# Optimization experiments

Measured on AMD Instinct MI355X. Metric: run time of the kernel, lower is better.

## Reference

```python
import jax, jax.numpy as jnp
import numpy as np

B, N, E, H = 16, 1024, 1024, 16
D = E // H  # head size = 64

def setup_inputs() -> dict:
    key = jax.random.key(0)
    ks = jax.random.split(key, 5)
    s = 1.0 / np.sqrt(E)
    return {
        "x": jax.random.normal(ks[0], (B, N, E), dtype=jnp.float32),
        "W_qkv": jax.random.normal(ks[1], (E, 3 * E), dtype=jnp.float32) * s,
        "b_qkv": jnp.zeros((3 * E,), dtype=jnp.float32),
        "W_proj": jax.random.normal(ks[2], (E, E), dtype=jnp.float32) * s,
        "b_proj": jnp.zeros((E,), dtype=jnp.float32),
    }

def reference(x, W_qkv, b_qkv, W_proj, b_proj):
    # qkv projection: [B,N,3E]
    qkv = x @ W_qkv + b_qkv
    q, k, v = jnp.split(qkv, 3, axis=-1)
    # b n (h d) -> b h n d
    def split_heads(t):
        return t.reshape(B, N, H, D).transpose(0, 2, 1, 3)
    q, k, v = split_heads(q), split_heads(k), split_heads(v)
    scale = D ** -0.5
    attn = jnp.einsum('bhnd,bhmd->bhnm', q, k) * scale  # [B,H,N,N]
    attn = jax.nn.softmax(attn, axis=-1)
    # dropout p=0 -> identity
    o = jnp.einsum('bhnm,bhmd->bhnd', attn, v)  # [B,H,N,D]
    o = o.transpose(0, 2, 1, 3).reshape(B, N, E)  # b h n d -> b n (h d)
    return o @ W_proj + b_proj
```

## Files before the change

kernel.cpp:

```cpp
#include <hip/hip_runtime.h>
#include <hip/hip_bf16.h>
#include <math.h>

#define BB 16
#define NN 1024
#define EE 1024
#define HH 16
#define DD 64
#define THREE_E 3072
#define M_TOTAL (BB * NN)

typedef __attribute__((ext_vector_type(8))) short bf16x8;
typedef __attribute__((ext_vector_type(4))) short bf16x4;
typedef __attribute__((ext_vector_type(4))) float floatx4;

#define SCALE_Q 0.18033688011112042f

static __device__ __forceinline__ unsigned short f2bf(float f) {
    union { float f; unsigned u; } x; x.f = f;
    unsigned r = x.u + 0x7fffu + ((x.u >> 16) & 1u);
    return (unsigned short)(r >> 16);
}

static __device__ __forceinline__ bf16x8 pack8v(floatx4 a, floatx4 b) {
    union { bf16x8 v; unsigned u[4]; } r;
    __hip_bfloat162 t;
    t = __float22bfloat162_rn(make_float2(a[0], a[1])); r.u[0] = *(unsigned*)&t;
    t = __float22bfloat162_rn(make_float2(a[2], a[3])); r.u[1] = *(unsigned*)&t;
    t = __float22bfloat162_rn(make_float2(b[0], b[1])); r.u[2] = *(unsigned*)&t;
    t = __float22bfloat162_rn(make_float2(b[2], b[3])); r.u[3] = *(unsigned*)&t;
    return r.v;
}
static __device__ __forceinline__ bf16x8 pack8f(float4 a, float4 b) {
    union { bf16x8 v; unsigned u[4]; } r;
    __hip_bfloat162 t;
    t = __float22bfloat162_rn(make_float2(a.x, a.y)); r.u[0] = *(unsigned*)&t;
    t = __float22bfloat162_rn(make_float2(a.z, a.w)); r.u[1] = *(unsigned*)&t;
    t = __float22bfloat162_rn(make_float2(b.x, b.y)); r.u[2] = *(unsigned*)&t;
    t = __float22bfloat162_rn(make_float2(b.z, b.w)); r.u[3] = *(unsigned*)&t;
    return r.v;
}

#define ASYNC16(gp, lp)                                                \
    __builtin_amdgcn_global_load_lds(                                  \
        (const __attribute__((address_space(1))) void*)(gp),           \
        (__attribute__((address_space(3))) void*)(lp), 16, 0, 0)

#define DRAIN_VMEM() __asm__ __volatile__("s_waitcnt vmcnt(0)" ::: "memory")

__global__ __launch_bounds__(256) void convert_x(
    const float* __restrict__ x, unsigned short* __restrict__ xb)
{
    int i = blockIdx.x * 256 + threadIdx.x;
    const float4* xp = (const float4*)x;
    float4 a = xp[i * 2], b = xp[i * 2 + 1];
    *(bf16x8*)&xb[i * 8] = pack8f(a, b);
}

__global__ __launch_bounds__(256) void wtrans(
    const float* __restrict__ w, unsigned short* __restrict__ wt, int R, int C)
{
    __shared__ float tile[32][33];
    const int t = threadIdx.x;
    const int lr = t >> 5, lc = t & 31;
    const int r0 = blockIdx.y * 32, c0 = blockIdx.x * 32;
    #pragma unroll
    for (int p = 0; p < 4; ++p)
        tile[lr + p * 8][lc] = w[(size_t)(r0 + lr + p * 8) * C + c0 + lc];
    __syncthreads();
    #pragma unroll
    for (int p = 0; p < 4; ++p) {
        int oc = lr + p * 8;
        float v = tile[lc][oc];
        wt[(size_t)(c0 + oc) * R + r0 + lc] = f2bf(v);
    }
}

__global__ __launch_bounds__(256) void gemm_qkv_mfma(
    const unsigned short* __restrict__ xb,
    const unsigned short* __restrict__ wt,
    const float* __restrict__ bias,
    unsigned short* __restrict__ Qo, unsigned short* __restrict__ Ko,
    unsigned short* __restrict__ Vo)
{
    __shared__ __align__(16) unsigned short As[128 * 32];
    __shared__ __align__(16) unsigned short Bs[128 * 32];

    const int t = threadIdx.x;
    const int w = t >> 6, lane = t & 63;
    const int quad = lane >> 4, l15 = lane & 15;
    const int wm = w >> 1, wn = w & 1;
    const int m0 = blockIdx.y * 128;
    const int n0 = blockIdx.x * 128;
    const int srow = lane >> 2;
    const int scw = (((lane & 3) ^ ((srow ^ (srow >> 2)) & 3))) * 8;
    const int rsw = ((quad ^ ((l15 ^ (l15 >> 2)) & 3))) * 8;

    floatx4 acc[4][4];
    #pragma unroll
    for (int i = 0; i < 4; ++i)
        #pragma unroll
        for (int j = 0; j < 4; ++j) acc[i][j] = (floatx4){0.f, 0.f, 0.f, 0.f};

    for (int kk = 0; kk < EE; kk += 32) {
        #pragma unroll
        for (int r = 0; r < 2; ++r) {
            int c = w * 2 + r;
            ASYNC16(&xb[(size_t)(m0 + c * 16 + srow) * EE + kk + scw],
                    &As[c * 512]);
            ASYNC16(&wt[(size_t)(n0 + c * 16 + srow) * EE + kk + scw],
                    &Bs[c * 512]);
        }
        DRAIN_VMEM();
        __syncthreads();

        bf16x8 af[4], bf[4];
        #pragma unroll
        for (int i = 0; i < 4; ++i) {
            af[i] = *(const bf16x8*)&As[(wm * 64 + i * 16 + l15) * 32 + rsw];
            bf[i] = *(const bf16x8*)&Bs[(wn * 64 + i * 16 + l15) * 32 + rsw];
        }
        #pragma unroll
        for (int i = 0; i < 4; ++i)
            #pragma unroll
            for (int j = 0; j < 4; ++j)
                acc[i][j] = __builtin_amdgcn_mfma_f32_16x16x32_bf16(
                    af[i], bf[j], acc[i][j], 0, 0, 0);
        __syncthreads();
    }

    const int mb = m0 + wm * 64;
    const int nb = n0 + wn * 64;
    #pragma unroll
    for (int i = 0; i < 4; ++i) {
        #pragma unroll
        for (int j = 0; j < 4; ++j) {
            int nc = nb + j * 16;
            int which = nc >> 10;
            int e0 = nc & 1023;
            int h  = e0 >> 6;
            int d0 = e0 & 63;
            float bv = bias[nc + l15];
            #pragma unroll
            for (int r = 0; r < 4; ++r) {
                int m = mb + i * 16 + quad * 4 + r;
                int b = m >> 10, n = m & 1023;
                size_t off = ((size_t)(b * HH + h) * NN + n) * DD + d0 + l15;
                float v = acc[i][j][r] + bv;
                if (which == 0)      Qo[off] = f2bf(v * SCALE_Q);
                else if (which == 1) Ko[off] = f2bf(v);
                else                 Vo[off] = f2bf(v);
            }
        }
    }
}

__global__ __launch_bounds__(256) void vtrans(
    const unsigned short* __restrict__ V, unsigned short* __restrict__ Vt)
{
    __shared__ __align__(16) unsigned short tile[64][72];
    const int t  = threadIdx.x;
    const int bh = blockIdx.x;
    const int n0 = blockIdx.y * 64;
    const int r  = t >> 2, c = t & 3;

    const unsigned short* src = &V[((size_t)bh * NN + n0 + r) * DD + c * 16];
    bf16x8 v0 = *(const bf16x8*)&src[0];
    bf16x8 v1 = *(const bf16x8*)&src[8];
    #pragma unroll
    for (int k = 0; k < 8; ++k) tile[c * 16 + k][r]     = v0[k];
    #pragma unroll
    for (int k = 0; k < 8; ++k) tile[c * 16 + 8 + k][r] = v1[k];
    __syncthreads();

    unsigned short* dst = &Vt[((size_t)bh * DD + r) * NN + n0 + c * 16];
    *(bf16x8*)&dst[0] = *(const bf16x8*)&tile[r][c * 16];
    *(bf16x8*)&dst[8] = *(const bf16x8*)&tile[r][c * 16 + 8];
}

__global__ __launch_bounds__(256) void attn_mfma(
    const unsigned short* __restrict__ Q,
    const unsigned short* __restrict__ K,
    const unsigned short* __restrict__ Vt,
    unsigned short* __restrict__ O)
{
    __shared__ __align__(16) unsigned short Ks[64 * 64];
    __shared__ __align__(16) unsigned short Vs[64 * 64];

    const int t    = threadIdx.x;
    const int w    = t >> 6;
    const int quad = (t >> 4) & 3;
    const int l15  = t & 15;
    const int i    = blockIdx.x;
    const int bh   = ((i >> 6) << 3) | (i & 7);
    const int qt   = (i >> 3) & 7;

    const unsigned short* Qg = Q  + (size_t)bh * NN * DD;
    const unsigned short* Kg = K  + (size_t)bh * NN * DD;
    const unsigned short* Vg = Vt + (size_t)bh * DD * NN;

    const int q0 = qt * 128 + w * 32;

    bf16x8 qf[2][2];
    #pragma unroll
    for (int a = 0; a < 2; ++a) {
        qf[a][0] = *(const bf16x8*)&Qg[(size_t)(q0 + a * 16 + l15) * DD + quad * 8];
        qf[a][1] = *(const bf16x8*)&Qg[(size_t)(q0 + a * 16 + l15) * DD + 32 + quad * 8];
    }

    floatx4 oa[2][4];
    #pragma unroll
    for (int a = 0; a < 2; ++a)
        #pragma unroll
        for (int jd = 0; jd < 4; ++jd) oa[a][jd] = (floatx4){0.f, 0.f, 0.f, 0.f};
    float lsum[2] = {0.f, 0.f};

    const int srow = t >> 2;
    const int sc   = t & 3;
    const int swz  = srow & 7;
    const int cbase = ((quad ^ (l15 & 7)) << 3);

    bf16x8 kr0, kr1, vr0, vr1;
    {
        const unsigned short* kg = &Kg[(size_t)srow * DD + sc * 16];
        kr0 = *(const bf16x8*)&kg[0];
        kr1 = *(const bf16x8*)&kg[8];
        const unsigned short* vg = &Vg[(size_t)srow * NN + sc * 16];
        vr0 = *(const bf16x8*)&vg[0];
        vr1 = *(const bf16x8*)&vg[8];
    }

    for (int kt = 0; kt < 16; ++kt) {
        __syncthreads();
        *(bf16x8*)&Ks[srow * 64 + (((2 * sc + 0) ^ swz) << 3)] = kr0;
        *(bf16x8*)&Ks[srow * 64 + (((2 * sc + 1) ^ swz) << 3)] = kr1;
        {
            bf16x4 h[4];
            h[0] = (bf16x4){vr0[0], vr0[1], vr0[2], vr0[3]};
            h[1] = (bf16x4){vr0[4], vr0[5], vr0[6], vr0[7]};
            h[2] = (bf16x4){vr1[0], vr1[1], vr1[2], vr1[3]};
            h[3] = (bf16x4){vr1[4], vr1[5], vr1[6], vr1[7]};
            #pragma unroll
            for (int q = 0; q < 4; ++q) {
                int col = ((((sc >> 1) * 4 + q) ^ swz) << 3) + ((sc & 1) << 2);
                *(bf16x4*)&Vs[srow * 64 + col] = h[q];
            }
        }
        __syncthreads();

        if (kt < 15) {
            const unsigned short* kg =
                &Kg[(size_t)((kt + 1) * 64 + srow) * DD + sc * 16];
            kr0 = *(const bf16x8*)&kg[0];
            kr1 = *(const bf16x8*)&kg[8];
            const unsigned short* vg =
                &Vg[(size_t)srow * NN + (kt + 1) * 64 + sc * 16];
            vr0 = *(const bf16x8*)&vg[0];
            vr1 = *(const bf16x8*)&vg[8];
        }

        floatx4 sa[2][4];
        #pragma unroll
        for (int a = 0; a < 2; ++a)
            #pragma unroll
            for (int tt = 0; tt < 4; ++tt) sa[a][tt] = (floatx4){0.f, 0.f, 0.f, 0.f};
        #pragma unroll
        for (int tt = 0; tt < 4; ++tt) {
            const unsigned short* kb = &Ks[(tt * 16 + l15) * 64];
            bf16x8 kf0 = *(const bf16x8*)&kb[cbase];
            bf16x8 kf1 = *(const bf16x8*)&kb[cbase ^ 32];
            #pragma unroll
            for (int a = 0; a < 2; ++a) {
                sa[a][tt] = __builtin_amdgcn_mfma_f32_16x16x32_bf16(
                    kf0, qf[a][0], sa[a][tt], 0, 0, 0);
                sa[a][tt] = __builtin_amdgcn_mfma_f32_16x16x32_bf16(
                    kf1, qf[a][1], sa[a][tt], 0, 0, 0);
            }
        }

        bf16x8 pf[2][2];
        #pragma unroll
        for (int a = 0; a < 2; ++a) {
            floatx4 pe[4];
            #pragma unroll
            for (int tt = 0; tt < 4; ++tt) {
                #pragma unroll
                for (int r = 0; r < 4; ++r) {
                    float p = exp2f(sa[a][tt][r]);
                    pe[tt][r] = p;
                    lsum[a] += p;
                }
            }
            pf[a][0] = pack8v(pe[0], pe[1]);
            pf[a][1] = pack8v(pe[2], pe[3]);
        }

        #pragma unroll
        for (int jd = 0; jd < 4; ++jd) {
            const unsigned short* vb = &Vs[(jd * 16 + l15) * 64];
            bf16x8 vf0 = *(const bf16x8*)&vb[cbase];
            bf16x8 vf1 = *(const bf16x8*)&vb[cbase ^ 32];
            #pragma unroll
            for (int a = 0; a < 2; ++a) {
                oa[a][jd] = __builtin_amdgcn_mfma_f32_16x16x32_bf16(
                    vf0, pf[a][0], oa[a][jd], 0, 0, 0);
                oa[a][jd] = __builtin_amdgcn_mfma_f32_16x16x32_bf16(
                    vf1, pf[a][1], oa[a][jd], 0, 0, 0);
            }
        }
    }

    #pragma unroll
    for (int a = 0; a < 2; ++a) {
        lsum[a] += __shfl_xor(lsum[a], 16, 64);
        lsum[a] += __shfl_xor(lsum[a], 32, 64);
    }

    const int b = bh >> 4, h = bh & 15;
    #pragma unroll
    for (int a = 0; a < 2; ++a) {
        float inv = 1.f / lsum[a];
        int n = q0 + a * 16 + l15;
        size_t base = (size_t)(b * NN + n) * EE + h * DD;
        #pragma unroll
        for (int jd = 0; jd < 4; ++jd) {
            bf16x4 v;
            v[0] = (short)f2bf(oa[a][jd][0] * inv);
            v[1] = (short)f2bf(oa[a][jd][1] * inv);
            v[2] = (short)f2bf(oa[a][jd][2] * inv);
            v[3] = (short)f2bf(oa[a][jd][3] * inv);
            *(bf16x4*)&O[base + jd * 16 + quad * 4] = v;
        }
    }
}

__global__ __launch_bounds__(256) void gemm_proj_mfma(
    const unsigned short* __restrict__ Ob,
    const unsigned short* __restrict__ Bp,
    const float* __restrict__ bias, float* __restrict__ out)
{
    __shared__ __align__(16) unsigned short As[128 * 32];
    __shared__ __align__(16) unsigned short Bs[128 * 32];

    const int t = threadIdx.x;
    const int w = t >> 6, lane = t & 63;
    const int quad = lane >> 4, l15 = lane & 15;
    const int wm = w >> 1, wn = w & 1;
    const int m0 = blockIdx.y * 128;
    const int n0 = blockIdx.x * 128;
    const int srow = lane >> 2;
    const int scw = (((lane & 3) ^ ((srow ^ (srow >> 2)) & 3))) * 8;
    const int rsw = ((quad ^ ((l15 ^ (l15 >> 2)) & 3))) * 8;

    floatx4 acc[4][4];
    #pragma unroll
    for (int i = 0; i < 4; ++i)
        #pragma unroll
        for (int j = 0; j < 4; ++j) acc[i][j] = (floatx4){0.f, 0.f, 0.f, 0.f};

    for (int kk = 0; kk < EE; kk += 32) {
        #pragma unroll
        for (int r = 0; r < 2; ++r) {
            int c = w * 2 + r;
            ASYNC16(&Ob[(size_t)(m0 + c * 16 + srow) * EE + kk + scw],
                    &As[c * 512]);
            ASYNC16(&Bp[(size_t)(n0 + c * 16 + srow) * EE + kk + scw],
                    &Bs[c * 512]);
        }
        DRAIN_VMEM();
        __syncthreads();

        bf16x8 af[4], bf[4];
        #pragma unroll
        for (int i = 0; i < 4; ++i) {
            af[i] = *(const bf16x8*)&As[(wm * 64 + i * 16 + l15) * 32 + rsw];
            bf[i] = *(const bf16x8*)&Bs[(wn * 64 + i * 16 + l15) * 32 + rsw];
        }
        #pragma unroll
        for (int i = 0; i < 4; ++i)
            #pragma unroll
            for (int j = 0; j < 4; ++j)
                acc[i][j] = __builtin_amdgcn_mfma_f32_16x16x32_bf16(
                    af[i], bf[j], acc[i][j], 0, 0, 0);
        __syncthreads();
    }

    const int mb = m0 + wm * 64;
    const int nb = n0 + wn * 64;
    #pragma unroll
    for (int i = 0; i < 4; ++i) {
        #pragma unroll
        for (int j = 0; j < 4; ++j) {
            float bv = bias[nb + j * 16 + l15];
            #pragma unroll
            for (int r = 0; r < 4; ++r) {
                int mrow = mb + i * 16 + quad * 4 + r;
                out[(size_t)mrow * EE + nb + j * 16 + l15] = acc[i][j][r] + bv;
            }
        }
    }
}

extern "C" void kernel_launch(void* const* d_in, const int* in_sizes, int n_in,
                              void* d_out, int out_size, void* d_ws, size_t ws_size,
                              hipStream_t stream) {
    const float* x     = (const float*)d_in[0];
    const float* Wqkv  = (const float*)d_in[1];
    const float* bqkv  = (const float*)d_in[2];
    const float* Wproj = (const float*)d_in[3];
    const float* bproj = (const float*)d_in[4];
    float* out = (float*)d_out;

    const size_t BHND = (size_t)BB * HH * NN * DD;
    unsigned short* Q   = (unsigned short*)d_ws;
    unsigned short* K   = Q   + BHND;
    unsigned short* Vn  = K   + BHND;
    unsigned short* Vt  = Vn  + BHND;
    unsigned short* Ob  = Vt  + BHND;
    unsigned short* xb  = Ob  + BHND;
    unsigned short* Wqt = xb  + BHND;
    unsigned short* Wpt = Wqt + (size_t)THREE_E * EE;

    dim3 blk(256);
    convert_x<<<dim3(M_TOTAL * EE / (256 * 8)), blk, 0, stream>>>(x, xb);
    wtrans<<<dim3(THREE_E / 32, EE / 32), blk, 0, stream>>>(Wqkv, Wqt, EE, THREE_E);
    wtrans<<<dim3(EE / 32, EE / 32), blk, 0, stream>>>(Wproj, Wpt, EE, EE);

    gemm_qkv_mfma<<<dim3(THREE_E / 128, M_TOTAL / 128), blk, 0, stream>>>(
        xb, Wqt, bqkv, Q, K, Vn);
    vtrans<<<dim3(BB * HH, NN / 64), blk, 0, stream>>>(Vn, Vt);
    attn_mfma<<<dim3(BB * HH * NN / 128), blk, 0, stream>>>(Q, K, Vt, Ob);
    gemm_proj_mfma<<<dim3(EE / 128, M_TOTAL / 128), blk, 0, stream>>>(
        Ob, Wpt, bproj, out);
}
```

Measured before the change: 447.2 us.

## Double GEMM K-tile, compute softmax row sums via MFMA, use raw exp2 and setprio

```diff
diff --git a/kernel.cpp b/kernel.cpp
--- a/kernel.cpp
+++ b/kernel.cpp
@@ -20,6 +20,14 @@
     union { float f; unsigned u; } x; x.f = f;
     unsigned r = x.u + 0x7fffu + ((x.u >> 16) & 1u);
     return (unsigned short)(r >> 16);
+}
+
+static __device__ __forceinline__ float fast_exp2(float x) {
+#if __has_builtin(__builtin_amdgcn_exp2f)
+    return __builtin_amdgcn_exp2f(x);
+#else
+    float r; __asm__("v_exp_f32 %0, %1" : "=v"(r) : "v"(x)); return r;
+#endif
 }
 
 static __device__ __forceinline__ bf16x8 pack8v(floatx4 a, floatx4 b) {
@@ -83,8 +91,8 @@
     unsigned short* __restrict__ Qo, unsigned short* __restrict__ Ko,
     unsigned short* __restrict__ Vo)
 {
-    __shared__ __align__(16) unsigned short As[128 * 32];
-    __shared__ __align__(16) unsigned short Bs[128 * 32];
+    __shared__ __align__(16) unsigned short As[128 * 64];
+    __shared__ __align__(16) unsigned short Bs[128 * 64];
 
     const int t = threadIdx.x;
     const int w = t >> 6, lane = t & 63;
@@ -92,9 +100,10 @@
     const int wm = w >> 1, wn = w & 1;
     const int m0 = blockIdx.y * 128;
     const int n0 = blockIdx.x * 128;
-    const int srow = lane >> 2;
-    const int scw = (((lane & 3) ^ ((srow ^ (srow >> 2)) & 3))) * 8;
-    const int rsw = ((quad ^ ((l15 ^ (l15 >> 2)) & 3))) * 8;
+    const int srow = lane >> 3;
+    const int sch  = lane & 7;
+    const int scw  = (sch ^ srow) * 8;
+    const int rb   = l15 & 7;
 
     floatx4 acc[4][4];
     #pragma unroll
@@ -102,30 +111,34 @@
         #pragma unroll
         for (int j = 0; j < 4; ++j) acc[i][j] = (floatx4){0.f, 0.f, 0.f, 0.f};
 
-    for (int kk = 0; kk < EE; kk += 32) {
-        #pragma unroll
-        for (int r = 0; r < 2; ++r) {
-            int c = w * 2 + r;
-            ASYNC16(&xb[(size_t)(m0 + c * 16 + srow) * EE + kk + scw],
-                    &As[c * 512]);
-            ASYNC16(&wt[(size_t)(n0 + c * 16 + srow) * EE + kk + scw],
-                    &Bs[c * 512]);
+    const unsigned short* aG = &xb[(size_t)(m0 + w * 8 + srow) * EE + scw];
+    const unsigned short* bG = &wt[(size_t)(n0 + w * 8 + srow) * EE + scw];
+
+    for (int kk = 0; kk < EE; kk += 64) {
+        #pragma unroll
+        for (int p = 0; p < 4; ++p) {
+            ASYNC16(aG + kk + (size_t)(p * 32) * EE, &As[(w * 8 + p * 32) * 64]);
+            ASYNC16(bG + kk + (size_t)(p * 32) * EE, &Bs[(w * 8 + p * 32) * 64]);
         }
         DRAIN_VMEM();
         __syncthreads();
 
-        bf16x8 af[4], bf[4];
-        #pragma unroll
-        for (int i = 0; i < 4; ++i) {
-            af[i] = *(const bf16x8*)&As[(wm * 64 + i * 16 + l15) * 32 + rsw];
-            bf[i] = *(const bf16x8*)&Bs[(wn * 64 + i * 16 + l15) * 32 + rsw];
-        }
-        #pragma unroll
-        for (int i = 0; i < 4; ++i)
-            #pragma unroll
-            for (int j = 0; j < 4; ++j)
-                acc[i][j] = __builtin_amdgcn_mfma_f32_16x16x32_bf16(
-                    af[i], bf[j], acc[i][j], 0, 0, 0);
+        #pragma unroll
+        for (int s = 0; s < 2; ++s) {
+            const int rsw = (((s << 2) | quad) ^ rb) * 8;
+            bf16x8 af[4], bf[4];
+            #pragma unroll
+            for (int i = 0; i < 4; ++i) {
+                af[i] = *(const bf16x8*)&As[(wm * 64 + i * 16 + l15) * 64 + rsw];
+                bf[i] = *(const bf16x8*)&Bs[(wn * 64 + i * 16 + l15) * 64 + rsw];
+            }
+            #pragma unroll
+            for (int i = 0; i < 4; ++i)
+                #pragma unroll
+                for (int j = 0; j < 4; ++j)
+                    acc[i][j] = __builtin_amdgcn_mfma_f32_16x16x32_bf16(
+                        af[i], bf[j], acc[i][j], 0, 0, 0);
+        }
         __syncthreads();
     }
 
@@ -208,12 +221,18 @@
         qf[a][1] = *(const bf16x8*)&Qg[(size_t)(q0 + a * 16 + l15) * DD + 32 + quad * 8];
     }
 
+    bf16x8 onesA;
+    #pragma unroll
+    for (int z = 0; z < 8; ++z) onesA[z] = (short)0x3F80;
+
     floatx4 oa[2][4];
     #pragma unroll
     for (int a = 0; a < 2; ++a)
         #pragma unroll
         for (int jd = 0; jd < 4; ++jd) oa[a][jd] = (floatx4){0.f, 0.f, 0.f, 0.f};
-    float lsum[2] = {0.f, 0.f};
+    floatx4 ls[2];
+    ls[0] = (floatx4){0.f, 0.f, 0.f, 0.f};
+    ls[1] = (floatx4){0.f, 0.f, 0.f, 0.f};
 
     const int srow = t >> 2;
     const int sc   = t & 3;
@@ -264,6 +283,7 @@
         for (int a = 0; a < 2; ++a)
             #pragma unroll
             for (int tt = 0; tt < 4; ++tt) sa[a][tt] = (floatx4){0.f, 0.f, 0.f, 0.f};
+        __builtin_amdgcn_s_setprio(1);
         #pragma unroll
         for (int tt = 0; tt < 4; ++tt) {
             const unsigned short* kb = &Ks[(tt * 16 + l15) * 64];
@@ -277,6 +297,7 @@
                     kf1, qf[a][1], sa[a][tt], 0, 0, 0);
             }
         }
+        __builtin_amdgcn_s_setprio(0);
 
         bf16x8 pf[2][2];
         #pragma unroll
@@ -285,16 +306,21 @@
             #pragma unroll
             for (int tt = 0; tt < 4; ++tt) {
                 #pragma unroll
-                for (int r = 0; r < 4; ++r) {
-                    float p = exp2f(sa[a][tt][r]);
-                    pe[tt][r] = p;
-                    lsum[a] += p;
-                }
+                for (int r = 0; r < 4; ++r)
+                    pe[tt][r] = fast_exp2(sa[a][tt][r]);
             }
             pf[a][0] = pack8v(pe[0], pe[1]);
             pf[a][1] = pack8v(pe[2], pe[3]);
         }
 
+        __builtin_amdgcn_s_setprio(1);
+        #pragma unroll
+        for (int a = 0; a < 2; ++a) {
+            ls[a] = __builtin_amdgcn_mfma_f32_16x16x32_bf16(
+                onesA, pf[a][0], ls[a], 0, 0, 0);
+            ls[a] = __builtin_amdgcn_mfma_f32_16x16x32_bf16(
+                onesA, pf[a][1], ls[a], 0, 0, 0);
+        }
         #pragma unroll
         for (int jd = 0; jd < 4; ++jd) {
             const unsigned short* vb = &Vs[(jd * 16 + l15) * 64];
@@ -308,18 +334,13 @@
                     vf1, pf[a][1], oa[a][jd], 0, 0, 0);
             }
         }
-    }
-
+        __builtin_amdgcn_s_setprio(0);
+    }
+
+    const int b = bh >> 4, h = bh & 15;
     #pragma unroll
     for (int a = 0; a < 2; ++a) {
-        lsum[a] += __shfl_xor(lsum[a], 16, 64);
-        lsum[a] += __shfl_xor(lsum[a], 32, 64);
-    }
-
-    const int b = bh >> 4, h = bh & 15;
-    #pragma unroll
-    for (int a = 0; a < 2; ++a) {
-        float inv = 1.f / lsum[a];
+        float inv = 1.f / ls[a][0];
         int n = q0 + a * 16 + l15;
         size_t base = (size_t)(b * NN + n) * EE + h * DD;
         #pragma unroll
@@ -339,8 +360,8 @@
     const unsigned short* __restrict__ Bp,
     const float* __restrict__ bias, float* __restrict__ out)
 {
-    __shared__ __align__(16) unsigned short As[128 * 32];
-    __shared__ __align__(16) unsigned short Bs[128 * 32];
+    __shared__ __align__(16) unsigned short As[128 * 64];
+    __shared__ __align__(16) unsigned short Bs[128 * 64];
 
     const int t = threadIdx.x;
     const int w = t >> 6, lane = t & 63;
@@ -348,9 +369,10 @@
     const int wm = w >> 1, wn = w & 1;
     const int m0 = blockIdx.y * 128;
     const int n0 = blockIdx.x * 128;
-    const int srow = lane >> 2;
-    const int scw = (((lane & 3) ^ ((srow ^ (srow >> 2)) & 3))) * 8;
-    const int rsw = ((quad ^ ((l15 ^ (l15 >> 2)) & 3))) * 8;
+    const int srow = lane >> 3;
+    const int sch  = lane & 7;
+    const int scw  = (sch ^ srow) * 8;
+    const int rb   = l15 & 7;
 
     floatx4 acc[4][4];
     #pragma unroll
@@ -358,30 +380,34 @@
         #pragma unroll
         for (int j = 0; j < 4; ++j) acc[i][j] = (floatx4){0.f, 0.f, 0.f, 0.f};
 
-    for (int kk = 0; kk < EE; kk += 32) {
-        #pragma unroll
-        for (int r = 0; r < 2; ++r) {
-            int c = w * 2 + r;
-            ASYNC16(&Ob[(size_t)(m0 + c * 16 + srow) * EE + kk + scw],
-                    &As[c * 512]);
-            ASYNC16(&Bp[(size_t)(n0 + c * 16 + srow) * EE + kk + scw],
-                    &Bs[c * 512]);
+    const unsigned short* aG = &Ob[(size_t)(m0 + w * 8 + srow) * EE + scw];
+    const unsigned short* bG = &Bp[(size_t)(n0 + w * 8 + srow) * EE + scw];
+
+    for (int kk = 0; kk < EE; kk += 64) {
+        #pragma unroll
+        for (int p = 0; p < 4; ++p) {
+            ASYNC16(aG + kk + (size_t)(p * 32) * EE, &As[(w * 8 + p * 32) * 64]);
+            ASYNC16(bG + kk + (size_t)(p * 32) * EE, &Bs[(w * 8 + p * 32) * 64]);
         }
         DRAIN_VMEM();
         __syncthreads();
 
-        bf16x8 af[4], bf[4];
-        #pragma unroll
-        for (int i = 0; i < 4; ++i) {
-            af[i] = *(const bf16x8*)&As[(wm * 64 + i * 16 + l15) * 32 + rsw];
-            bf[i] = *(const bf16x8*)&Bs[(wn * 64 + i * 16 + l15) * 32 + rsw];
-        }
-        #pragma unroll
-        for (int i = 0; i < 4; ++i)
-            #pragma unroll
-            for (int j = 0; j < 4; ++j)
-                acc[i][j] = __builtin_amdgcn_mfma_f32_16x16x32_bf16(
-                    af[i], bf[j], acc[i][j], 0, 0, 0);
+        #pragma unroll
+        for (int s = 0; s < 2; ++s) {
+            const int rsw = (((s << 2) | quad) ^ rb) * 8;
+            bf16x8 af[4], bf[4];
+            #pragma unroll
+            for (int i = 0; i < 4; ++i) {
+                af[i] = *(const bf16x8*)&As[(wm * 64 + i * 16 + l15) * 64 + rsw];
+                bf[i] = *(const bf16x8*)&Bs[(wn * 64 + i * 16 + l15) * 64 + rsw];
+            }
+            #pragma unroll
+            for (int i = 0; i < 4; ++i)
+                #pragma unroll
+                for (int j = 0; j < 4; ++j)
+                    acc[i][j] = __builtin_amdgcn_mfma_f32_16x16x32_bf16(
+                        af[i], bf[j], acc[i][j], 0, 0, 0);
+        }
         __syncthreads();
     }
 
```

After: 404.5 us. -9.5%, faster.
